# Performance work log

Hardware: AMD Instinct MI355X
Metric: run time of the kernel (lower is better)

Reference implementation:

```python
import jax, jax.numpy as jnp
import numpy as np

K = 20
HID = 64
NUM_CLASSES = 50
BIG = 1e10  # effectively-infinite distance for self-loop exclusion


def knn_idx(x, k):
    # x: [N, d] -> idx: [N, k] indices of k nearest neighbors in feature space (excluding self)
    sq = jnp.sum(x * x, axis=1)
    dist = sq[:, None] + sq[None, :] - 2.0 * (x @ x.T)  # [N, N]
    n = x.shape[0]
    dist = dist.at[jnp.arange(n), jnp.arange(n)].set(BIG)
    _, idx = jax.lax.top_k(-dist, k)
    return idx


def edge_conv(x, k, W, b):
    # DynamicEdgeConv: message = relu(Linear(cat[x_i, x_j - x_i])), aggr = max over k neighbors
    idx = knn_idx(x, k)                      # [N, k]
    xj = x[idx]                              # [N, k, d] neighbor gather
    xi = jnp.broadcast_to(x[:, None, :], xj.shape)
    feat = jnp.concatenate([xi, xj - xi], axis=-1)   # [N, k, 2d]
    h = jax.nn.relu(jnp.einsum('nkf,fo->nko', feat, W) + b)
    return jnp.max(h, axis=1)                # [N, out]


def setup_inputs() -> dict:
    key = jax.random.key(0)
    ks = jax.random.split(key, 16)
    def lin(kw, fan_in, fan_out):
        s = 1.0 / np.sqrt(fan_in)
        return jax.random.uniform(kw, (fan_in, fan_out), jnp.float32, -s, s)
    inp = {
        'x':  jax.random.normal(ks[0], (8192, 3), jnp.float32),
        'W1': lin(ks[1], 2 * 3, HID),      'b1': jnp.zeros((HID,), jnp.float32),
        'W2': lin(ks[2], 2 * HID, HID),    'b2': jnp.zeros((HID,), jnp.float32),
        'W3': lin(ks[3], 2 * HID, HID),    'b3': jnp.zeros((HID,), jnp.float32),
        'Wl': lin(ks[4], 3 * HID, 1024),   'bl': jnp.zeros((1024,), jnp.float32),
        'Wm1': lin(ks[5], 1024, 256),      'bm1': jnp.zeros((256,), jnp.float32),
        'Wm2': lin(ks[6], 256, 128),       'bm2': jnp.zeros((128,), jnp.float32),
        'Wo': lin(ks[7], 128, NUM_CLASSES),'bo': jnp.zeros((NUM_CLASSES,), jnp.float32),
    }
    return inp


def reference(x, W1, b1, W2, b2, W3, b3, Wl, bl, Wm1, bm1, Wm2, bm2, Wo, bo):
    x1 = edge_conv(x, K, W1, b1)     # [N, 64], kNN on raw 3-D points
    x2 = edge_conv(x1, K, W2, b2)    # [N, 64], kNN recomputed in feature space
    x3 = edge_conv(x2, K, W3, b3)    # [N, 64]
    h = jnp.concatenate([x1, x2, x3], axis=1)            # [N, 192]
    h = jax.nn.relu(h @ Wl + bl)                         # lin1: MLP([192, 1024])
    h = jax.nn.relu(h @ Wm1 + bm1)                       # MLP([1024, 256]) (dropout: eval mode)
    h = jax.nn.relu(h @ Wm2 + bm2)                       # MLP([256, 128])
    out = h @ Wo + bo                                    # final Linear
    return jax.nn.log_softmax(out, axis=-1)
```

## Files before the change

### kernel.cpp

```cpp
#include <hip/hip_runtime.h>
#include <math.h>

#define NPTS 8192
#define KNN 20
#define NLISTS 32

#define OFF_SQ   0
#define OFF_IDX  8192
#define OFF_A    172032
#define OFF_B    696320
#define OFF_CAT  1220608
#define OFF_H1   2793472
#define OFF_H2   11182080
#define OFF_H3   13279232
#define OFF_PART OFF_H1
#define OFF_PACK (OFF_H1 + 5242880)
#define PACK_ELEMS 262144
#define OFF_WT   OFF_A

typedef __attribute__((ext_vector_type(8))) short bf16x8;
typedef __attribute__((ext_vector_type(16))) float f32x16;

__device__ inline unsigned umed3(unsigned a, unsigned b, unsigned c) {
    unsigned d;
    asm("v_med3_u32 %0, %1, %2, %3" : "=v"(d) : "v"(a), "v"(b), "v"(c));
    return d;
}

__device__ inline unsigned short f2bf(float f) {
    unsigned u = __float_as_uint(f);
    u += 0x7FFFu + ((u >> 16) & 1u);
    return (unsigned short)(u >> 16);
}

template<int D>
__global__ __launch_bounds__(256)
void sqnorm_kernel(const float* __restrict__ X, int stride, float* __restrict__ sq) {
    int n = blockIdx.x * blockDim.x + threadIdx.x;
    if (n < NPTS) {
        float s = 0.f;
        #pragma unroll
        for (int f = 0; f < D; ++f) {
            float v = X[(size_t)n * stride + f];
            s = fmaf(v, v, s);
        }
        sq[n] = s;
    }
}

template<int D, int KP>
__global__ __launch_bounds__(256)
void prepack_kernel(const float* __restrict__ X, int stride,
                    unsigned short* __restrict__ Xhi, unsigned short* __restrict__ Xlo,
                    unsigned short* __restrict__ Yhi, unsigned short* __restrict__ Ylo) {
    int t2 = blockIdx.x * 256 + threadIdx.x;
    int t = t2 * 2;
    int n = t >> (KP == 64 ? 6 : 4);
    int k = t & (KP - 1);
    float xv[2];
    xv[0] = (k     < D) ? X[(size_t)n * stride + k]     : 0.f;
    xv[1] = (k + 1 < D) ? X[(size_t)n * stride + k + 1] : 0.f;
    ushort2 hx, lx, hy, ly;
    unsigned short* hxp = (unsigned short*)&hx;
    unsigned short* lxp = (unsigned short*)&lx;
    unsigned short* hyp = (unsigned short*)&hy;
    unsigned short* lyp = (unsigned short*)&ly;
    #pragma unroll
    for (int e = 0; e < 2; ++e) {
        float x = xv[e];
        unsigned short hi = f2bf(x);
        float hif = __uint_as_float((unsigned)hi << 16);
        unsigned short lo = f2bf(x - hif);
        float y = -2.f * x;
        unsigned short yhi = f2bf(y);
        float yhif = __uint_as_float((unsigned)yhi << 16);
        unsigned short ylo = f2bf(y - yhif);
        hxp[e] = hi; lxp[e] = lo; hyp[e] = yhi; lyp[e] = ylo;
    }
    *(ushort2*)&Xhi[t] = hx;
    *(ushort2*)&Xlo[t] = lx;
    *(ushort2*)&Yhi[t] = hy;
    *(ushort2*)&Ylo[t] = ly;
}

template<int K, int NBITS>
__global__ __launch_bounds__(256)
void prepack_w(const float* __restrict__ W,
               unsigned short* __restrict__ Thi, unsigned short* __restrict__ Tlo) {
    const int N = 1 << NBITS;
    int t = blockIdx.x * 256 + threadIdx.x;
    int k = t >> NBITS, n = t & (N - 1);
    float x = W[t];
    unsigned short hi = f2bf(x);
    float hif = __uint_as_float((unsigned)hi << 16);
    unsigned short lo = f2bf(x - hif);
    Thi[(size_t)n * K + k] = hi;
    Tlo[(size_t)n * K + k] = lo;
}

#define PROCESS(Cv, j0base)                                                    \
    do {                                                                       \
        _Pragma("unroll")                                                      \
        for (int q = 0; q < 4; ++q) {                                          \
            _Pragma("unroll")                                                  \
            for (int t = 0; t < 4; ++t) {                                      \
                const int j = (j0base) + h * 4 + q * 8 + t;                    \
                float dd = fmaxf((Cv)[q * 4 + t], 0.f);                        \
                unsigned key = (__float_as_uint(dd) & 0xFFFFE000u) | (unsigned)j; \
                if (j == bi) key = 0xFFFFFFFFu;                                \
                _Pragma("unroll")                                              \
                for (int p = KNN - 1; p >= 1; --p)                             \
                    top[p] = umed3(key, top[p - 1], top[p]);                   \
                top[0] = min(top[0], key);                                     \
            }                                                                  \
        }                                                                      \
    } while (0)

template<int KP>
__global__ __launch_bounds__(256, 2)
void knnA_mfma(const unsigned short* __restrict__ Yhi, const unsigned short* __restrict__ Ylo,
               const unsigned short* __restrict__ Xhi, const unsigned short* __restrict__ Xlo,
               const float* __restrict__ sq, unsigned int* __restrict__ part) {
    constexpr int NS = KP / 16;
    constexpr int NT = 8;
    const int wave = threadIdx.x >> 6, lane = threadIdx.x & 63;
    const int col = lane & 31;
    const int h   = lane >> 5;
    const int bi  = (blockIdx.x * 4 + wave) * 32 + col;
    const int jbase = blockIdx.y * 256;

    bf16x8 bhi[NS], blo[NS];
    #pragma unroll
    for (int s = 0; s < NS; ++s) {
        bhi[s] = *(const bf16x8*)&Xhi[(size_t)bi * KP + s * 16 + h * 8];
        blo[s] = *(const bf16x8*)&Xlo[(size_t)bi * KP + s * 16 + h * 8];
    }
    const float sqi = sq[bi];

    unsigned top[KNN];
    #pragma unroll
    for (int k = 0; k < KNN; ++k) top[k] = 0xFFFFFFFFu;

    bf16x8 fA[NS], fB[NS], lo[NS];
    f32x16 CCa, CCb;

    {
        const size_t a0 = (size_t)(jbase + col) * KP + h * 8;
        #pragma unroll
        for (int s = 0; s < NS; ++s)
            fA[s] = *(const bf16x8*)&Yhi[a0 + s * 16];
    }

    #pragma unroll 1
    for (int jt2 = 0; jt2 < NT; jt2 += 2) {
        const int j0 = jbase + jt2 * 32;
        const int aj = j0 + col;

        #pragma unroll
        for (int s = 0; s < NS; ++s)
            fB[s] = *(const bf16x8*)&Yhi[(size_t)(aj + 32) * KP + s * 16 + h * 8];
        #pragma unroll
        for (int s = 0; s < NS; ++s)
            lo[s] = *(const bf16x8*)&Ylo[(size_t)aj * KP + s * 16 + h * 8];
        float4 e0 = *(const float4*)&sq[j0 + h * 4];
        float4 e1 = *(const float4*)&sq[j0 + h * 4 + 8];
        float4 e2 = *(const float4*)&sq[j0 + h * 4 + 16];
        float4 e3 = *(const float4*)&sq[j0 + h * 4 + 24];

        if (jt2 > 0) PROCESS(CCb, j0 - 32);

        CCa[0] = sqi + e0.x; CCa[1] = sqi + e0.y; CCa[2]  = sqi + e0.z; CCa[3]  = sqi + e0.w;
        CCa[4] = sqi + e1.x; CCa[5] = sqi + e1.y; CCa[6]  = sqi + e1.z; CCa[7]  = sqi + e1.w;
        CCa[8] = sqi + e2.x; CCa[9] = sqi + e2.y; CCa[10] = sqi + e2.z; CCa[11] = sqi + e2.w;
        CCa[12] = sqi + e3.x; CCa[13] = sqi + e3.y; CCa[14] = sqi + e3.z; CCa[15] = sqi + e3.w;
        #pragma unroll
        for (int s = 0; s < NS; ++s) {
            CCa = __builtin_amdgcn_mfma_f32_32x32x16_bf16(fA[s], bhi[s], CCa, 0, 0, 0);
            CCa = __builtin_amdgcn_mfma_f32_32x32x16_bf16(fA[s], blo[s], CCa, 0, 0, 0);
            CCa = __builtin_amdgcn_mfma_f32_32x32x16_bf16(lo[s], bhi[s], CCa, 0, 0, 0);
        }

        if (jt2 + 2 < NT) {
            #pragma unroll
            for (int s = 0; s < NS; ++s)
                fA[s] = *(const bf16x8*)&Yhi[(size_t)(aj + 64) * KP + s * 16 + h * 8];
        }
        #pragma unroll
        for (int s = 0; s < NS; ++s)
            lo[s] = *(const bf16x8*)&Ylo[(size_t)(aj + 32) * KP + s * 16 + h * 8];
        float4 o0 = *(const float4*)&sq[j0 + 32 + h * 4];
        float4 o1 = *(const float4*)&sq[j0 + 32 + h * 4 + 8];
        float4 o2 = *(const float4*)&sq[j0 + 32 + h * 4 + 16];
        float4 o3 = *(const float4*)&sq[j0 + 32 + h * 4 + 24];

        PROCESS(CCa, j0);

        CCb[0] = sqi + o0.x; CCb[1] = sqi + o0.y; CCb[2]  = sqi + o0.z; CCb[3]  = sqi + o0.w;
        CCb[4] = sqi + o1.x; CCb[5] = sqi + o1.y; CCb[6]  = sqi + o1.z; CCb[7]  = sqi + o1.w;
        CCb[8] = sqi + o2.x; CCb[9] = sqi + o2.y; CCb[10] = sqi + o2.z; CCb[11] = sqi + o2.w;
        CCb[12] = sqi + o3.x; CCb[13] = sqi + o3.y; CCb[14] = sqi + o3.z; CCb[15] = sqi + o3.w;
        #pragma unroll
        for (int s = 0; s < NS; ++s) {
            CCb = __builtin_amdgcn_mfma_f32_32x32x16_bf16(fB[s], bhi[s], CCb, 0, 0, 0);
            CCb = __builtin_amdgcn_mfma_f32_32x32x16_bf16(fB[s], blo[s], CCb, 0, 0, 0);
            CCb = __builtin_amdgcn_mfma_f32_32x32x16_bf16(lo[s], bhi[s], CCb, 0, 0, 0);
        }
    }
    PROCESS(CCb, jbase + (NT - 1) * 32);

    {
        bool done = false;
        #pragma unroll
        for (int k = 0; k < KNN; ++k) {
            unsigned c = __shfl_xor(top[k], 32);
            if (!done) done = __all(c >= top[KNN - 1]);
            if (!done) {
                #pragma unroll
                for (int p = KNN - 1; p >= 1; --p)
                    top[p] = umed3(c, top[p - 1], top[p]);
                top[0] = min(top[0], c);
            }
        }
    }

    if (h == 0) {
        unsigned* o = part + ((size_t)bi * NLISTS + blockIdx.y) * KNN;
        #pragma unroll
        for (int k = 0; k < KNN; ++k) o[k] = top[k];
    }
}

__global__ __launch_bounds__(256)
void knnB_kernel(const unsigned int* __restrict__ part, int* __restrict__ idx_out) {
    const int wave = threadIdx.x >> 6, lane = threadIdx.x & 63;
    const int half = lane >> 5;
    const int l = lane & 31;
    const int row = (blockIdx.x * 4 + wave) * 2 + half;

    unsigned top[KNN];
    const unsigned* p = part + ((size_t)row * NLISTS + l) * KNN;
    #pragma unroll
    for (int k = 0; k < KNN; k += 4) {
        uint4 v = *(const uint4*)(p + k);
        top[k] = v.x; top[k + 1] = v.y; top[k + 2] = v.z; top[k + 3] = v.w;
    }

    #pragma unroll
    for (int mi = 0; mi < 5; ++mi) {
        const int m = 1 << mi;
        bool done = false;
        #pragma unroll
        for (int k = 0; k < KNN; ++k) {
            unsigned c = __shfl_xor(top[k], m);
            if (!done) done = __all(c >= top[KNN - 1]);
            if (!done) {
                #pragma unroll
                for (int q = KNN - 1; q >= 1; --q)
                    top[q] = umed3(c, top[q - 1], top[q]);
                top[0] = min(top[0], c);
            }
        }
    }

    if (l == 0) {
        #pragma unroll
        for (int k = 0; k < KNN; ++k)
            idx_out[(size_t)row * KNN + k] = (int)(top[k] & 0x1FFFu);
    }
}

template<int D>
__global__ __launch_bounds__(256)
void featAB_kernel(const float* __restrict__ X, int stride, const float* __restrict__ W,
                   float* __restrict__ A, float* __restrict__ B) {
    const int wave = threadIdx.x >> 6, lane = threadIdx.x & 63;
    const int n = blockIdx.x * 4 + wave;
    float a = 0.f, b = 0.f;
    const float* xp = X + (size_t)n * stride;
    #pragma unroll
    for (int f = 0; f < D; ++f) {
        float xf = xp[f];
        a = fmaf(xf, W[(size_t)f * 64 + lane], a);
        b = fmaf(xf, W[(size_t)(D + f) * 64 + lane], b);
    }
    A[(size_t)n * 64 + lane] = a;
    B[(size_t)n * 64 + lane] = b;
}

__global__ __launch_bounds__(256)
void edge_fuse_kernel(const float* __restrict__ A, const float* __restrict__ B,
                      const int* __restrict__ idx, const float* __restrict__ bias,
                      float* __restrict__ out, int ostride,
                      float* __restrict__ sqo,
                      unsigned short* __restrict__ Xhi, unsigned short* __restrict__ Xlo,
                      unsigned short* __restrict__ Yhi, unsigned short* __restrict__ Ylo) {
    const int wave = threadIdx.x >> 6, lane = threadIdx.x & 63;
    const int n = blockIdx.x * 4 + wave;
    const float base = A[(size_t)n * 64 + lane] - B[(size_t)n * 64 + lane] + bias[lane];
    float m = -INFINITY;
    #pragma unroll 4
    for (int k = 0; k < KNN; ++k) {
        int j = idx[(size_t)n * KNN + k];
        m = fmaxf(m, base + B[(size_t)j * 64 + lane]);
    }
    m = fmaxf(m, 0.f);
    out[(size_t)n * ostride + lane] = m;

    float s = m * m;
    #pragma unroll
    for (int off = 32; off; off >>= 1) s += __shfl_xor(s, off);
    if (lane == 0) sqo[n] = s;

    unsigned short hi = f2bf(m);
    float hif = __uint_as_float((unsigned)hi << 16);
    unsigned short lo = f2bf(m - hif);
    float y = -2.f * m;
    unsigned short yhi = f2bf(y);
    float yhif = __uint_as_float((unsigned)yhi << 16);
    unsigned short ylo = f2bf(y - yhif);
    Xhi[(size_t)n * 64 + lane] = hi;
    Xlo[(size_t)n * 64 + lane] = lo;
    Yhi[(size_t)n * 64 + lane] = yhi;
    Ylo[(size_t)n * 64 + lane] = ylo;
}

__global__ __launch_bounds__(256)
void edge_agg_kernel(const float* __restrict__ A, const float* __restrict__ B,
                     const int* __restrict__ idx, const float* __restrict__ bias,
                     float* __restrict__ out, int ostride) {
    const int wave = threadIdx.x >> 6, lane = threadIdx.x & 63;
    const int n = blockIdx.x * 4 + wave;
    const float base = A[(size_t)n * 64 + lane] - B[(size_t)n * 64 + lane] + bias[lane];
    float m = -INFINITY;
    #pragma unroll 4
    for (int k = 0; k < KNN; ++k) {
        int j = idx[(size_t)n * KNN + k];
        m = fmaxf(m, base + B[(size_t)j * 64 + lane]);
    }
    out[(size_t)n * ostride + lane] = fmaxf(m, 0.f);
}

template<int K, int N, int CTW>
__global__ __launch_bounds__(256, 3)
void gemm_mfma_relu(const float* __restrict__ A,
                    const unsigned short* __restrict__ Whi, const unsigned short* __restrict__ Wlo,
                    const float* __restrict__ bias, float* __restrict__ C) {
    const int wave = threadIdx.x >> 6, lane = threadIdx.x & 63;
    const int col = lane & 31, h = lane >> 5;
    const int r0 = blockIdx.x * 32;
    const int nb = blockIdx.y * (CTW * 128) + wave * (CTW * 32);
    const float* arow = A + (size_t)(r0 + col) * K + h * 8;

    f32x16 acc[CTW];
    #pragma unroll
    for (int c = 0; c < CTW; ++c)
        #pragma unroll
        for (int r = 0; r < 16; ++r) acc[c][r] = 0.f;

    #pragma unroll 4
    for (int s = 0; s < K / 16; ++s) {
        float4 f0 = *(const float4*)(arow + s * 16);
        float4 f1 = *(const float4*)(arow + s * 16 + 4);
        bf16x8 ahi, alo;
        {
            float xv[8] = {f0.x, f0.y, f0.z, f0.w, f1.x, f1.y, f1.z, f1.w};
            #pragma unroll
            for (int e = 0; e < 8; ++e) {
                unsigned u = __float_as_uint(xv[e]);
                ahi[e] = (short)(u >> 16);
                float d = xv[e] - __uint_as_float(u & 0xFFFF0000u);
                alo[e] = (short)(__float_as_uint(d) >> 16);
            }
        }
        #pragma unroll
        for (int c = 0; c < CTW; ++c) {
            const size_t wb = (size_t)(nb + c * 32 + col) * K + s * 16 + h * 8;
            bf16x8 bhi = *(const bf16x8*)&Whi[wb];
            bf16x8 blo = *(const bf16x8*)&Wlo[wb];
            acc[c] = __builtin_amdgcn_mfma_f32_32x32x16_bf16(ahi, bhi, acc[c], 0, 0, 0);
            acc[c] = __builtin_amdgcn_mfma_f32_32x32x16_bf16(alo, bhi, acc[c], 0, 0, 0);
            acc[c] = __builtin_amdgcn_mfma_f32_32x32x16_bf16(ahi, blo, acc[c], 0, 0, 0);
        }
    }

    #pragma unroll
    for (int c = 0; c < CTW; ++c) {
        const int n = nb + c * 32 + col;
        const float b = bias[n];
        #pragma unroll
        for (int q = 0; q < 4; ++q)
            #pragma unroll
            for (int t = 0; t < 4; ++t) {
                const int rl = 4 * h + 8 * q + t;
                C[(size_t)(r0 + rl) * N + n] = fmaxf(acc[c][q * 4 + t] + b, 0.f);
            }
    }
}

__global__ __launch_bounds__(256)
void final_kernel(const float* __restrict__ H, const float* __restrict__ Wo,
                  const float* __restrict__ bo, float* __restrict__ out) {
    const int wave = threadIdx.x >> 6, lane = threadIdx.x & 63;
    const int n = blockIdx.x * 4 + wave;
    float v = -INFINITY;
    if (lane < 50) {
        float a = bo[lane];
        const float* h = H + (size_t)n * 128;
        #pragma unroll 4
        for (int f = 0; f < 128; ++f) a = fmaf(h[f], Wo[f * 50 + lane], a);
        v = a;
    }
    float mx = v;
    #pragma unroll
    for (int off = 32; off; off >>= 1) mx = fmaxf(mx, __shfl_xor(mx, off));
    float e = (lane < 50) ? expf(v - mx) : 0.f;
    float s = e;
    #pragma unroll
    for (int off = 32; off; off >>= 1) s += __shfl_xor(s, off);
    if (lane < 50) out[(size_t)n * 50 + lane] = v - mx - logf(s);
}

extern "C" void kernel_launch(void* const* d_in, const int* in_sizes, int n_in,
                              void* d_out, int out_size, void* d_ws, size_t ws_size,
                              hipStream_t stream) {
    const float* x   = (const float*)d_in[0];
    const float* W1  = (const float*)d_in[1];
    const float* b1  = (const float*)d_in[2];
    const float* W2  = (const float*)d_in[3];
    const float* b2  = (const float*)d_in[4];
    const float* W3  = (const float*)d_in[5];
    const float* b3  = (const float*)d_in[6];
    const float* Wl  = (const float*)d_in[7];
    const float* bl  = (const float*)d_in[8];
    const float* Wm1 = (const float*)d_in[9];
    const float* bm1 = (const float*)d_in[10];
    const float* Wm2 = (const float*)d_in[11];
    const float* bm2 = (const float*)d_in[12];
    const float* Wo  = (const float*)d_in[13];
    const float* bo  = (const float*)d_in[14];

    float* ws   = (float*)d_ws;
    float* sq   = ws + OFF_SQ;
    int*   idx  = (int*)(ws + OFF_IDX);
    float* Abuf = ws + OFF_A;
    float* Bbuf = ws + OFF_B;
    float* cat  = ws + OFF_CAT;
    float* h1   = ws + OFF_H1;
    unsigned int* part = (unsigned int*)(ws + OFF_PART);
    unsigned short* Phi = (unsigned short*)(ws + OFF_PACK);
    unsigned short* Plo = (unsigned short*)(ws + OFF_PACK + PACK_ELEMS);
    unsigned short* Qhi = (unsigned short*)(ws + OFF_PACK + 2 * PACK_ELEMS);
    unsigned short* Qlo = (unsigned short*)(ws + OFF_PACK + 3 * PACK_ELEMS);
    float* h2   = ws + OFF_H2;
    float* h3   = ws + OFF_H3;
    unsigned short* WlT_hi  = (unsigned short*)(ws + OFF_WT);
    unsigned short* WlT_lo  = (unsigned short*)(ws + OFF_WT + 98304);
    unsigned short* Wm1T_hi = (unsigned short*)(ws + OFF_WT + 196608);
    unsigned short* Wm1T_lo = (unsigned short*)(ws + OFF_WT + 327680);
    unsigned short* Wm2T_hi = (unsigned short*)(ws + OFF_WT + 458752);
    unsigned short* Wm2T_lo = (unsigned short*)(ws + OFF_WT + 475136);
    float* out  = (float*)d_out;

    dim3 b256(256);
    dim3 gknn(64, 32);

    sqnorm_kernel<3><<<32, b256, 0, stream>>>(x, 3, sq);
    prepack_kernel<3, 16><<<256, b256, 0, stream>>>(x, 3, Phi, Plo, Qhi, Qlo);
    knnA_mfma<16><<<gknn, b256, 0, stream>>>(Qhi, Qlo, Phi, Plo, sq, part);
    knnB_kernel<<<1024, b256, 0, stream>>>(part, idx);
    featAB_kernel<3><<<2048, b256, 0, stream>>>(x, 3, W1, Abuf, Bbuf);
    edge_fuse_kernel<<<2048, b256, 0, stream>>>(Abuf, Bbuf, idx, b1, cat + 0, 192,
                                                sq, Phi, Plo, Qhi, Qlo);

    knnA_mfma<64><<<gknn, b256, 0, stream>>>(Qhi, Qlo, Phi, Plo, sq, part);
    knnB_kernel<<<1024, b256, 0, stream>>>(part, idx);
    featAB_kernel<64><<<2048, b256, 0, stream>>>(cat + 0, 192, W2, Abuf, Bbuf);
    edge_fuse_kernel<<<2048, b256, 0, stream>>>(Abuf, Bbuf, idx, b2, cat + 64, 192,
                                                sq, Phi, Plo, Qhi, Qlo);

    knnA_mfma<64><<<gknn, b256, 0, stream>>>(Qhi, Qlo, Phi, Plo, sq, part);
    knnB_kernel<<<1024, b256, 0, stream>>>(part, idx);
    featAB_kernel<64><<<2048, b256, 0, stream>>>(cat + 64, 192, W3, Abuf, Bbuf);
    edge_agg_kernel<<<2048, b256, 0, stream>>>(Abuf, Bbuf, idx, b3, cat + 128, 192);

    prepack_w<192, 10><<<768, b256, 0, stream>>>(Wl, WlT_hi, WlT_lo);
    prepack_w<1024, 8><<<1024, b256, 0, stream>>>(Wm1, Wm1T_hi, Wm1T_lo);
    prepack_w<256, 7><<<128, b256, 0, stream>>>(Wm2, Wm2T_hi, Wm2T_lo);

    dim3 g1(256, 4);
    gemm_mfma_relu<192, 1024, 2><<<g1, b256, 0, stream>>>(cat, WlT_hi, WlT_lo, bl, h1);
    dim3 g2(256, 1);
    gemm_mfma_relu<1024, 256, 2><<<g2, b256, 0, stream>>>(h1, Wm1T_hi, Wm1T_lo, bm1, h2);
    dim3 g3(256, 1);
    gemm_mfma_relu<256, 128, 1><<<g3, b256, 0, stream>>>(h2, Wm2T_hi, Wm2T_lo, bm2, h3);
    final_kernel<<<2048, b256, 0, stream>>>(h3, Wo, bo, out);
}
```

Measured before the change: 519.1 us.

## Fuse small launches and emit pre-split bf16 hi/lo activations for MLP GEMMs

Merges sqnorm and x prepacking into one setup kernel, merges knnB with featAB into one launch, and combines the three weight prepacks into one kernel, which cuts launch count. Edge aggregation and GEMM epilogues now write activations already split into bf16 hi/lo pairs, so the next GEMM loads them directly instead of converting fp32 in its inner loop. The Wm1 GEMM grid changes to two column blocks with one tile per wave. This adds extra hi/lo stores and workspace aliasing (catHi shares space with h2hi) that must not overlap in time.

```diff
diff --git a/kernel.cpp b/kernel.cpp
--- a/kernel.cpp
+++ b/kernel.cpp
@@ -33,67 +33,69 @@
     return (unsigned short)(u >> 16);
 }
 
-template<int D>
+__device__ inline void tsplit(float x, unsigned short& hi, unsigned short& lo) {
+    unsigned u = __float_as_uint(x);
+    hi = (unsigned short)(u >> 16);
+    float d = x - __uint_as_float(u & 0xFFFF0000u);
+    lo = (unsigned short)(__float_as_uint(d) >> 16);
+}
+
 __global__ __launch_bounds__(256)
-void sqnorm_kernel(const float* __restrict__ X, int stride, float* __restrict__ sq) {
-    int n = blockIdx.x * blockDim.x + threadIdx.x;
-    if (n < NPTS) {
-        float s = 0.f;
-        #pragma unroll
-        for (int f = 0; f < D; ++f) {
-            float v = X[(size_t)n * stride + f];
-            s = fmaf(v, v, s);
-        }
-        sq[n] = s;
-    }
-}
-
-template<int D, int KP>
+void setup_kernel(const float* __restrict__ x, float* __restrict__ sq,
+                  unsigned short* __restrict__ Xhi, unsigned short* __restrict__ Xlo,
+                  unsigned short* __restrict__ Yhi, unsigned short* __restrict__ Ylo) {
+    const int b = blockIdx.x;
+    if (b < 256) {
+        int t = (b * 256 + threadIdx.x) * 2;
+        int n = t >> 4, k = t & 15;
+        float xv[2];
+        xv[0] = (k < 3) ? x[(size_t)n * 3 + k] : 0.f;
+        xv[1] = (k + 1 < 3) ? x[(size_t)n * 3 + k + 1] : 0.f;
+        ushort2 hx, lx, hy, ly;
+        unsigned short* hxp = (unsigned short*)&hx;
+        unsigned short* lxp = (unsigned short*)&lx;
+        unsigned short* hyp = (unsigned short*)&hy;
+        unsigned short* lyp = (unsigned short*)&ly;
+        #pragma unroll
+        for (int e = 0; e < 2; ++e) {
+            float xx = xv[e];
+            unsigned short hi = f2bf(xx);
+            float hif = __uint_as_float((unsigned)hi << 16);
+            unsigned short lo = f2bf(xx - hif);
+            float y = -2.f * xx;
+            unsigned short yhi = f2bf(y);
+            float yhif = __uint_as_float((unsigned)yhi << 16);
+            unsigned short ylo = f2bf(y - yhif);
+            hxp[e] = hi; lxp[e] = lo; hyp[e] = yhi; lyp[e] = ylo;
+        }
+        *(ushort2*)&Xhi[t] = hx;
+        *(ushort2*)&Xlo[t] = lx;
+        *(ushort2*)&Yhi[t] = hy;
+        *(ushort2*)&Ylo[t] = ly;
+    } else {
+        int n = (b - 256) * 256 + threadIdx.x;
+        float a = x[(size_t)n * 3], bb = x[(size_t)n * 3 + 1], c = x[(size_t)n * 3 + 2];
+        sq[n] = fmaf(a, a, fmaf(bb, bb, c * c));
+    }
+}
+
 __global__ __launch_bounds__(256)
-void prepack_kernel(const float* __restrict__ X, int stride,
-                    unsigned short* __restrict__ Xhi, unsigned short* __restrict__ Xlo,
-                    unsigned short* __restrict__ Yhi, unsigned short* __restrict__ Ylo) {
-    int t2 = blockIdx.x * 256 + threadIdx.x;
-    int t = t2 * 2;
-    int n = t >> (KP == 64 ? 6 : 4);
-    int k = t & (KP - 1);
-    float xv[2];
-    xv[0] = (k     < D) ? X[(size_t)n * stride + k]     : 0.f;
-    xv[1] = (k + 1 < D) ? X[(size_t)n * stride + k + 1] : 0.f;
-    ushort2 hx, lx, hy, ly;
-    unsigned short* hxp = (unsigned short*)&hx;
-    unsigned short* lxp = (unsigned short*)&lx;
-    unsigned short* hyp = (unsigned short*)&hy;
-    unsigned short* lyp = (unsigned short*)&ly;
-    #pragma unroll
-    for (int e = 0; e < 2; ++e) {
-        float x = xv[e];
-        unsigned short hi = f2bf(x);
-        float hif = __uint_as_float((unsigned)hi << 16);
-        unsigned short lo = f2bf(x - hif);
-        float y = -2.f * x;
-        unsigned short yhi = f2bf(y);
-        float yhif = __uint_as_float((unsigned)yhi << 16);
-        unsigned short ylo = f2bf(y - yhif);
-        hxp[e] = hi; lxp[e] = lo; hyp[e] = yhi; lyp[e] = ylo;
-    }
-    *(ushort2*)&Xhi[t] = hx;
-    *(ushort2*)&Xlo[t] = lx;
-    *(ushort2*)&Yhi[t] = hy;
-    *(ushort2*)&Ylo[t] = ly;
-}
-
-template<int K, int NBITS>
-__global__ __launch_bounds__(256)
-void prepack_w(const float* __restrict__ W,
-               unsigned short* __restrict__ Thi, unsigned short* __restrict__ Tlo) {
-    const int N = 1 << NBITS;
-    int t = blockIdx.x * 256 + threadIdx.x;
-    int k = t >> NBITS, n = t & (N - 1);
-    float x = W[t];
-    unsigned short hi = f2bf(x);
+void wprep_kernel(const float* __restrict__ Wl, const float* __restrict__ Wm1,
+                  const float* __restrict__ Wm2,
+                  unsigned short* __restrict__ WlT_hi, unsigned short* __restrict__ WlT_lo,
+                  unsigned short* __restrict__ Wm1T_hi, unsigned short* __restrict__ Wm1T_lo,
+                  unsigned short* __restrict__ Wm2T_hi, unsigned short* __restrict__ Wm2T_lo) {
+    const int b = blockIdx.x;
+    const float* W; unsigned short *Thi, *Tlo; int t, K, nmask, nbits;
+    if (b < 768)       { W = Wl;  Thi = WlT_hi;  Tlo = WlT_lo;  t = b * 256 + threadIdx.x;          K = 192;  nbits = 10; }
+    else if (b < 1792) { W = Wm1; Thi = Wm1T_hi; Tlo = Wm1T_lo; t = (b - 768) * 256 + threadIdx.x;  K = 1024; nbits = 8; }
+    else               { W = Wm2; Thi = Wm2T_hi; Tlo = Wm2T_lo; t = (b - 1792) * 256 + threadIdx.x; K = 256;  nbits = 7; }
+    nmask = (1 << nbits) - 1;
+    int k = t >> nbits, n = t & nmask;
+    float xx = W[t];
+    unsigned short hi = f2bf(xx);
     float hif = __uint_as_float((unsigned)hi << 16);
-    unsigned short lo = f2bf(x - hif);
+    unsigned short lo = f2bf(xx - hif);
     Thi[(size_t)n * K + k] = hi;
     Tlo[(size_t)n * K + k] = lo;
 }
@@ -230,67 +232,68 @@
     }
 }
 
-__global__ __launch_bounds__(256)
-void knnB_kernel(const unsigned int* __restrict__ part, int* __restrict__ idx_out) {
-    const int wave = threadIdx.x >> 6, lane = threadIdx.x & 63;
-    const int half = lane >> 5;
-    const int l = lane & 31;
-    const int row = (blockIdx.x * 4 + wave) * 2 + half;
-
-    unsigned top[KNN];
-    const unsigned* p = part + ((size_t)row * NLISTS + l) * KNN;
-    #pragma unroll
-    for (int k = 0; k < KNN; k += 4) {
-        uint4 v = *(const uint4*)(p + k);
-        top[k] = v.x; top[k + 1] = v.y; top[k + 2] = v.z; top[k + 3] = v.w;
-    }
-
-    #pragma unroll
-    for (int mi = 0; mi < 5; ++mi) {
-        const int m = 1 << mi;
-        bool done = false;
-        #pragma unroll
-        for (int k = 0; k < KNN; ++k) {
-            unsigned c = __shfl_xor(top[k], m);
-            if (!done) done = __all(c >= top[KNN - 1]);
-            if (!done) {
-                #pragma unroll
-                for (int q = KNN - 1; q >= 1; --q)
-                    top[q] = umed3(c, top[q - 1], top[q]);
-                top[0] = min(top[0], c);
-            }
-        }
-    }
-
-    if (l == 0) {
-        #pragma unroll
-        for (int k = 0; k < KNN; ++k)
-            idx_out[(size_t)row * KNN + k] = (int)(top[k] & 0x1FFFu);
-    }
-}
-
 template<int D>
 __global__ __launch_bounds__(256)
-void featAB_kernel(const float* __restrict__ X, int stride, const float* __restrict__ W,
-                   float* __restrict__ A, float* __restrict__ B) {
+void knnBfeat_kernel(const unsigned int* __restrict__ part, int* __restrict__ idx_out,
+                     const float* __restrict__ X, int stride, const float* __restrict__ W,
+                     float* __restrict__ A, float* __restrict__ B) {
     const int wave = threadIdx.x >> 6, lane = threadIdx.x & 63;
-    const int n = blockIdx.x * 4 + wave;
-    float a = 0.f, b = 0.f;
-    const float* xp = X + (size_t)n * stride;
-    #pragma unroll
-    for (int f = 0; f < D; ++f) {
-        float xf = xp[f];
-        a = fmaf(xf, W[(size_t)f * 64 + lane], a);
-        b = fmaf(xf, W[(size_t)(D + f) * 64 + lane], b);
-    }
-    A[(size_t)n * 64 + lane] = a;
-    B[(size_t)n * 64 + lane] = b;
-}
-
+    if (blockIdx.x < 1024) {
+        const int half = lane >> 5;
+        const int l = lane & 31;
+        const int row = (blockIdx.x * 4 + wave) * 2 + half;
+
+        unsigned top[KNN];
+        const unsigned* p = part + ((size_t)row * NLISTS + l) * KNN;
+        #pragma unroll
+        for (int k = 0; k < KNN; k += 4) {
+            uint4 v = *(const uint4*)(p + k);
+            top[k] = v.x; top[k + 1] = v.y; top[k + 2] = v.z; top[k + 3] = v.w;
+        }
+
+        #pragma unroll
+        for (int mi = 0; mi < 5; ++mi) {
+            const int m = 1 << mi;
+            bool done = false;
+            #pragma unroll
+            for (int k = 0; k < KNN; ++k) {
+                unsigned c = __shfl_xor(top[k], m);
+                if (!done) done = __all(c >= top[KNN - 1]);
+                if (!done) {
+                    #pragma unroll
+                    for (int q = KNN - 1; q >= 1; --q)
+                        top[q] = umed3(c, top[q - 1], top[q]);
+                    top[0] = min(top[0], c);
+                }
+            }
+        }
+
+        if (l == 0) {
+            #pragma unroll
+            for (int k = 0; k < KNN; ++k)
+                idx_out[(size_t)row * KNN + k] = (int)(top[k] & 0x1FFFu);
+        }
+    } else {
+        const int n = (blockIdx.x - 1024) * 4 + wave;
+        float a = 0.f, b = 0.f;
+        const float* xp = X + (size_t)n * stride;
+        #pragma unroll
+        for (int f = 0; f < D; ++f) {
+            float xf = xp[f];
+            a = fmaf(xf, W[(size_t)f * 64 + lane], a);
+            b = fmaf(xf, W[(size_t)(D + f) * 64 + lane], b);
+        }
+        A[(size_t)n * 64 + lane] = a;
+        B[(size_t)n * 64 + lane] = b;
+    }
+}
+
+template<bool PACKS>
 __global__ __launch_bounds__(256)
 void edge_fuse_kernel(const float* __restrict__ A, const float* __restrict__ B,
                       const int* __restrict__ idx, const float* __restrict__ bias,
-                      float* __restrict__ out, int ostride,
+                      float* __restrict__ out, int colofs,
+                      unsigned short* __restrict__ catHi, unsigned short* __restrict__ catLo,
                       float* __restrict__ sqo,
                       unsigned short* __restrict__ Xhi, unsigned short* __restrict__ Xlo,
                       unsigned short* __restrict__ Yhi, unsigned short* __restrict__ Ylo) {
@@ -304,52 +307,44 @@
         m = fmaxf(m, base + B[(size_t)j * 64 + lane]);
     }
     m = fmaxf(m, 0.f);
-    out[(size_t)n * ostride + lane] = m;
-
-    float s = m * m;
-    #pragma unroll
-    for (int off = 32; off; off >>= 1) s += __shfl_xor(s, off);
-    if (lane == 0) sqo[n] = s;
-
-    unsigned short hi = f2bf(m);
-    float hif = __uint_as_float((unsigned)hi << 16);
-    unsigned short lo = f2bf(m - hif);
-    float y = -2.f * m;
-    unsigned short yhi = f2bf(y);
-    float yhif = __uint_as_float((unsigned)yhi << 16);
-    unsigned short ylo = f2bf(y - yhif);
-    Xhi[(size_t)n * 64 + lane] = hi;
-    Xlo[(size_t)n * 64 + lane] = lo;
-    Yhi[(size_t)n * 64 + lane] = yhi;
-    Ylo[(size_t)n * 64 + lane] = ylo;
-}
-
-__global__ __launch_bounds__(256)
-void edge_agg_kernel(const float* __restrict__ A, const float* __restrict__ B,
-                     const int* __restrict__ idx, const float* __restrict__ bias,
-                     float* __restrict__ out, int ostride) {
-    const int wave = threadIdx.x >> 6, lane = threadIdx.x & 63;
-    const int n = blockIdx.x * 4 + wave;
-    const float base = A[(size_t)n * 64 + lane] - B[(size_t)n * 64 + lane] + bias[lane];
-    float m = -INFINITY;
-    #pragma unroll 4
-    for (int k = 0; k < KNN; ++k) {
-        int j = idx[(size_t)n * KNN + k];
-        m = fmaxf(m, base + B[(size_t)j * 64 + lane]);
-    }
-    out[(size_t)n * ostride + lane] = fmaxf(m, 0.f);
-}
-
-template<int K, int N, int CTW>
+    out[(size_t)n * 192 + colofs + lane] = m;
+
+    unsigned short chi, clo;
+    tsplit(m, chi, clo);
+    catHi[(size_t)n * 192 + colofs + lane] = chi;
+    catLo[(size_t)n * 192 + colofs + lane] = clo;
+
+    if constexpr (PACKS) {
+        float s = m * m;
+        #pragma unroll
+        for (int off = 32; off; off >>= 1) s += __shfl_xor(s, off);
+        if (lane == 0) sqo[n] = s;
+
+        unsigned short hi = f2bf(m);
+        float hif = __uint_as_float((unsigned)hi << 16);
+        unsigned short lo = f2bf(m - hif);
+        float y = -2.f * m;
+        unsigned short yhi = f2bf(y);
+        float yhif = __uint_as_float((unsigned)yhi << 16);
+        unsigned short ylo = f2bf(y - yhif);
+        Xhi[(size_t)n * 64 + lane] = hi;
+        Xlo[(size_t)n * 64 + lane] = lo;
+        Yhi[(size_t)n * 64 + lane] = yhi;
+        Ylo[(size_t)n * 64 + lane] = ylo;
+    }
+}
+
+template<int K, int N, int CTW, bool SPLIT_OUT>
 __global__ __launch_bounds__(256, 3)
-void gemm_mfma_relu(const float* __restrict__ A,
-                    const unsigned short* __restrict__ Whi, const unsigned short* __restrict__ Wlo,
-                    const float* __restrict__ bias, float* __restrict__ C) {
+void gemm_mfma(const unsigned short* __restrict__ Ahi, const unsigned short* __restrict__ Alo,
+               const unsigned short* __restrict__ Whi, const unsigned short* __restrict__ Wlo,
+               const float* __restrict__ bias, float* __restrict__ C,
+               unsigned short* __restrict__ Chi, unsigned short* __restrict__ Clo) {
     const int wave = threadIdx.x >> 6, lane = threadIdx.x & 63;
     const int col = lane & 31, h = lane >> 5;
     const int r0 = blockIdx.x * 32;
     const int nb = blockIdx.y * (CTW * 128) + wave * (CTW * 32);
-    const float* arow = A + (size_t)(r0 + col) * K + h * 8;
+    const size_t abase = (size_t)(r0 + col) * K + h * 8;
 
     f32x16 acc[CTW];
     #pragma unroll
@@ -359,19 +354,8 @@
 
     #pragma unroll 4
     for (int s = 0; s < K / 16; ++s) {
-        float4 f0 = *(const float4*)(arow + s * 16);
-        float4 f1 = *(const float4*)(arow + s * 16 + 4);
-        bf16x8 ahi, alo;
-        {
-            float xv[8] = {f0.x, f0.y, f0.z, f0.w, f1.x, f1.y, f1.z, f1.w};
-            #pragma unroll
-            for (int e = 0; e < 8; ++e) {
-                unsigned u = __float_as_uint(xv[e]);
-                ahi[e] = (short)(u >> 16);
-                float d = xv[e] - __uint_as_float(u & 0xFFFF0000u);
-                alo[e] = (short)(__float_as_uint(d) >> 16);
-            }
-        }
+        bf16x8 ahi = *(const bf16x8*)&Ahi[abase + s * 16];
+        bf16x8 alo = *(const bf16x8*)&Alo[abase + s * 16];
         #pragma unroll
         for (int c = 0; c < CTW; ++c) {
             const size_t wb = (size_t)(nb + c * 32 + col) * K + s * 16 + h * 8;
@@ -392,7 +376,15 @@
             #pragma unroll
             for (int t = 0; t < 4; ++t) {
                 const int rl = 4 * h + 8 * q + t;
-                C[(size_t)(r0 + rl) * N + n] = fmaxf(acc[c][q * 4 + t] + b, 0.f);
+                float v = fmaxf(acc[c][q * 4 + t] + b, 0.f);
+                if constexpr (SPLIT_OUT) {
+                    unsigned short vh, vl;
+                    tsplit(v, vh, vl);
+                    Chi[(size_t)(r0 + rl) * N + n] = vh;
+                    Clo[(size_t)(r0 + rl) * N + n] = vl;
+                } else {
+                    C[(size_t)(r0 + rl) * N + n] = v;
+                }
             }
     }
 }
@@ -445,13 +437,17 @@
     float* Abuf = ws + OFF_A;
     float* Bbuf = ws + OFF_B;
     float* cat  = ws + OFF_CAT;
-    float* h1   = ws + OFF_H1;
     unsigned int* part = (unsigned int*)(ws + OFF_PART);
     unsigned short* Phi = (unsigned short*)(ws + OFF_PACK);
     unsigned short* Plo = (unsigned short*)(ws + OFF_PACK + PACK_ELEMS);
     unsigned short* Qhi = (unsigned short*)(ws + OFF_PACK + 2 * PACK_ELEMS);
     unsigned short* Qlo = (unsigned short*)(ws + OFF_PACK + 3 * PACK_ELEMS);
-    float* h2   = ws + OFF_H2;
+    unsigned short* h1hi = (unsigned short*)(ws + OFF_H1);
+    unsigned short* h1lo = (unsigned short*)(ws + OFF_H1 + 4194304);
+    unsigned short* catHi = (unsigned short*)(ws + OFF_H2);
+    unsigned short* catLo = (unsigned short*)(ws + OFF_H2 + 786432);
+    unsigned short* h2hi = (unsigned short*)(ws + OFF_H2);
+    unsigned short* h2lo = (unsigned short*)(ws + OFF_H2 + 1048576);
     float* h3   = ws + OFF_H3;
     unsigned short* WlT_hi  = (unsigned short*)(ws + OFF_WT);
     unsigned short* WlT_lo  = (unsigned short*)(ws + OFF_WT + 98304);
@@ -464,34 +460,34 @@
     dim3 b256(256);
     dim3 gknn(64, 32);
 
-    sqnorm_kernel<3><<<32, b256, 0, stream>>>(x, 3, sq);
-    prepack_kernel<3, 16><<<256, b256, 0, stream>>>(x, 3, Phi, Plo, Qhi, Qlo);
+    setup_kernel<<<288, b256, 0, stream>>>(x, sq, Phi, Plo, Qhi, Qlo);
     knnA_mfma<16><<<gknn, b256, 0, stream>>>(Qhi, Qlo, Phi, Plo, sq, part);
-    knnB_kernel<<<1024, b256, 0, stream>>>(part, idx);
-    featAB_kernel<3><<<2048, b256, 0, stream>>>(x, 3, W1, Abuf, Bbuf);
-    edge_fuse_kernel<<<2048, b256, 0, stream>>>(Abuf, Bbuf, idx, b1, cat + 0, 192,
-                                                sq, Phi, Plo, Qhi, Qlo);
+    knnBfeat_kernel<3><<<3072, b256, 0, stream>>>(part, idx, x, 3, W1, Abuf, Bbuf);
+    edge_fuse_kernel<true><<<2048, b256, 0, stream>>>(Abuf, Bbuf, idx, b1, cat, 0,
+                                                      catHi, catLo, sq, Phi, Plo, Qhi, Qlo);
 
     knnA_mfma<64><<<gknn, b256, 0, stream>>>(Qhi, Qlo, Phi, Plo, sq, part);
-    knnB_kernel<<<1024, b256, 0, stream>>>(part, idx);
-    featAB_kernel<64><<<2048, b256, 0, stream>>>(cat + 0, 192, W2, Abuf, Bbuf);
-    edge_fuse_kernel<<<2048, b256, 0, stream>>>(Abuf, Bbuf, idx, b2, cat + 64, 192,
-                                                sq, Phi, Plo, Qhi, Qlo);
+    knnBfeat_kernel<64><<<3072, b256, 0, stream>>>(part, idx, cat, 192, W2, Abuf, Bbuf);
+    edge_fuse_kernel<true><<<2048, b256, 0, stream>>>(Abuf, Bbuf, idx, b2, cat, 64,
+                                                      catHi, catLo, sq, Phi, Plo, Qhi, Qlo);
 
     knnA_mfma<64><<<gknn, b256, 0, stream>>>(Qhi, Qlo, Phi, Plo, sq, part);
-    knnB_kernel<<<1024, b256, 0, stream>>>(part, idx);
-    featAB_kernel<64><<<2048, b256, 0, stream>>>(cat + 64, 192, W3, Abuf, Bbuf);
-    edge_agg_kernel<<<2048, b256, 0, stream>>>(Abuf, Bbuf, idx, b3, cat + 128, 192);
-
-    prepack_w<192, 10><<<768, b256, 0, stream>>>(Wl, WlT_hi, WlT_lo);
-    prepack_w<1024, 8><<<1024, b256, 0, stream>>>(Wm1, Wm1T_hi, Wm1T_lo);
-    prepack_w<256, 7><<<128, b256, 0, stream>>>(Wm2, Wm2T_hi, Wm2T_lo);
+    knnBfeat_kernel<64><<<3072, b256, 0, stream>>>(part, idx, cat + 64, 192, W3, Abuf, Bbuf);
+    edge_fuse_kernel<false><<<2048, b256, 0, stream>>>(Abuf, Bbuf, idx, b3, cat, 128,
+                                                       catHi, catLo, nullptr,
+                                                       nullptr, nullptr, nullptr, nullptr);
+
+    wprep_kernel<<<1920, b256, 0, stream>>>(Wl, Wm1, Wm2, WlT_hi, WlT_lo,
+                                            Wm1T_hi, Wm1T_lo, Wm2T_hi, Wm2T_lo);
 
     dim3 g1(256, 4);
-    gemm_mfma_relu<192, 1024, 2><<<g1, b256, 0, stream>>>(cat, WlT_hi, WlT_lo, bl, h1);
-    dim3 g2(256, 1);
-    gemm_mfma_relu<1024, 256, 2><<<g2, b256, 0, stream>>>(h1, Wm1T_hi, Wm1T_lo, bm1, h2);
+    gemm_mfma<192, 1024, 2, true><<<g1, b256, 0, stream>>>(catHi, catLo, WlT_hi, WlT_lo,
+                                                           bl, nullptr, h1hi, h1lo);
+    dim3 g2(256, 2);
+    gemm_mfma<1024, 256, 1, true><<<g2, b256, 0, stream>>>(h1hi, h1lo, Wm1T_hi, Wm1T_lo,
+                                                           bm1, nullptr, h2hi, h2lo);
     dim3 g3(256, 1);
-    gemm_mfma_relu<256, 128, 1><<<g3, b256, 0, stream>>>(h2, Wm2T_hi, Wm2T_lo, bm2, h3);
+    gemm_mfma<256, 128, 1, false><<<g3, b256, 0, stream>>>(h2hi, h2lo, Wm2T_hi, Wm2T_lo,
+                                                           bm2, h3, nullptr, nullptr);
     final_kernel<<<2048, b256, 0, stream>>>(h3, Wo, bo, out);
 }
```

Result: faster. 472.1 us (-9.1%).
